# Kernel tuning notes

Measured on AMD Instinct MI355X. Metric: run time of the kernel, lower is better.

## Reference

```python
import jax, jax.numpy as jnp
import numpy as np

B, T, C = 4, 2048, 1024
H = 16
D = C // H  # head_dim = 64


def setup_inputs() -> dict:
    key = jax.random.key(0)
    ks = jax.random.split(key, 9)
    s = 1.0 / np.sqrt(C)
    return {
        "x": jax.random.normal(ks[0], (B, T, C), dtype=jnp.float32),
        "wq": jax.random.uniform(ks[1], (C, C), jnp.float32, -s, s),
        "bq": jax.random.uniform(ks[2], (C,), jnp.float32, -s, s),
        "wk": jax.random.uniform(ks[3], (C, C), jnp.float32, -s, s),
        "bk": jax.random.uniform(ks[4], (C,), jnp.float32, -s, s),
        "wv": jax.random.uniform(ks[5], (C, C), jnp.float32, -s, s),
        "bv": jax.random.uniform(ks[6], (C,), jnp.float32, -s, s),
        "wo": jax.random.uniform(ks[7], (C, C), jnp.float32, -s, s),
        "bo": jax.random.uniform(ks[8], (C,), jnp.float32, -s, s),
    }


def reference(x, wq, bq, wk, bk, wv, bv, wo, bo):
    # Linear layers (torch convention: y = x @ W.T + b)
    q = x @ wq.T + bq  # [B,T,C]
    k = x @ wk.T + bk
    v = x @ wv.T + bv
    # split heads -> [B,H,T,D]
    q = q.reshape(B, T, H, D).transpose(0, 2, 1, 3)
    k = k.reshape(B, T, H, D).transpose(0, 2, 1, 3)
    v = v.reshape(B, T, H, D).transpose(0, 2, 1, 3)
    scores = jnp.einsum('bhqd,bhkd->bhqk', q, k) / jnp.sqrt(jnp.float32(D))
    causal = jnp.tril(jnp.ones((T, T), dtype=bool))  # position i attends to j<=i
    scores = jnp.where(causal, scores, -jnp.inf)
    attn = jax.nn.softmax(scores, axis=-1)
    # dropout p=0.0 (eval / identity)
    out = jnp.einsum('bhqk,bhkd->bhqd', attn, v)  # [B,H,T,D]
    out = out.transpose(0, 2, 1, 3).reshape(B, T, C)
    return out @ wo.T + bo
```

## Files before the change

kernel.cpp:

```cpp
#include <hip/hip_runtime.h>
#include <stdint.h>

#define B_DIM 4
#define T_DIM 2048
#define C_DIM 1024
#define H_DIM 16
#define D_DIM 64
#define M_DIM (B_DIM * T_DIM)
#define QK_SCALE 0.18033688011112042f

typedef float f32x4 __attribute__((ext_vector_type(4)));
typedef float f32x16 __attribute__((ext_vector_type(16)));
typedef short bf16x8 __attribute__((ext_vector_type(8)));
typedef unsigned short u16;
typedef u16 u16x8 __attribute__((ext_vector_type(8)));

static __device__ __forceinline__ u16 f2b(float f) {
  uint32_t r;
  asm("v_cvt_pk_bf16_f32 %0, %1, %1" : "=v"(r) : "v"(f));
  return (u16)r;
}
static __device__ __forceinline__ uint32_t f2b2(float a, float b) {
  uint32_t r;
  asm("v_cvt_pk_bf16_f32 %0, %1, %2" : "=v"(r) : "v"(a), "v"(b));
  return r;
}
static __device__ __forceinline__ float xhalf_max(float x) {
  return fmaxf(x, __shfl_xor(x, 32, 64));
}
static __device__ __forceinline__ float xhalf_sum(float x) {
  return x + __shfl_xor(x, 32, 64);
}

static __device__ __forceinline__ void gl_lds16(const u16* g, u16* l) {
  __builtin_amdgcn_global_load_lds(
      (const __attribute__((address_space(1))) void*)g,
      (__attribute__((address_space(3))) void*)l, 16, 0, 0);
}

__global__ void k_cvt_all(const float* __restrict__ x,
                          const float* __restrict__ s0, const float* __restrict__ s1,
                          const float* __restrict__ s2, const float* __restrict__ s3,
                          u16* __restrict__ dx,
                          u16* __restrict__ d0, u16* __restrict__ d1,
                          u16* __restrict__ d2, u16* __restrict__ d3) {
  int i = blockIdx.x * blockDim.x + threadIdx.x;
  const float* s;
  u16* d;
  int j;
  if (i < (1 << 21)) {
    s = x; d = dx; j = i;
  } else {
    int k = i - (1 << 21);
    int seg = k >> 18;
    j = k & ((1 << 18) - 1);
    s = seg == 0 ? s0 : seg == 1 ? s1 : seg == 2 ? s2 : s3;
    d = seg == 0 ? d0 : seg == 1 ? d1 : seg == 2 ? d2 : d3;
  }
  float4 v = ((const float4*)s)[j];
  uint2 o;
  o.x = f2b2(v.x, v.y);
  o.y = f2b2(v.z, v.w);
  ((uint2*)d)[j] = o;
}

__global__ __launch_bounds__(256) void k_gemm_qkv(
    const u16* __restrict__ A,
    const u16* __restrict__ w0, const u16* __restrict__ w1, const u16* __restrict__ w2,
    const float* __restrict__ b0, const float* __restrict__ b1, const float* __restrict__ b2,
    u16* __restrict__ Qo, u16* __restrict__ Ko, u16* __restrict__ Vto) {
  __shared__ u16 As[128 * 32];
  __shared__ u16 Bs[128 * 32];
  const int tid = threadIdx.x;
  const int l = tid & 63;
  const int w = tid >> 6;
  const int wr = w >> 1, wc = w & 1;
  const int seg = blockIdx.x >> 3;
  const int brow = blockIdx.y * 128, bcol = (blockIdx.x & 7) * 128;
  const int lrow = l & 15, lk = l >> 4;
  const int K = C_DIM;

  const u16* Bw = seg == 0 ? w0 : seg == 1 ? w1 : w2;
  const float* bias = seg == 0 ? b0 : seg == 1 ? b1 : b2;
  const float scale = seg == 0 ? QK_SCALE : 1.f;

  f32x4 acc[4][4];
  for (int m = 0; m < 4; ++m)
    for (int n = 0; n < 4; ++n)
      acc[m][n] = (f32x4){0.f, 0.f, 0.f, 0.f};

  for (int kt = 0; kt < K; kt += 32) {
    __syncthreads();
    {
      int slot = tid;
      int r0 = slot >> 2, c0 = slot & 3;
      gl_lds16(A + (size_t)(brow + r0) * K + kt + c0 * 8, As + slot * 8);
      gl_lds16(Bw + (size_t)(bcol + r0) * K + kt + c0 * 8, Bs + slot * 8);
      int slot2 = slot + 256;
      int r1 = slot2 >> 2, c1 = slot2 & 3;
      gl_lds16(A + (size_t)(brow + r1) * K + kt + c1 * 8, As + slot2 * 8);
      gl_lds16(Bw + (size_t)(bcol + r1) * K + kt + c1 * 8, Bs + slot2 * 8);
    }
    asm volatile("s_waitcnt vmcnt(0)" ::: "memory");
    __syncthreads();

    bf16x8 af[4], bfr[4];
#pragma unroll
    for (int m = 0; m < 4; ++m)
      af[m] = *(const bf16x8*)(As + (wr * 64 + m * 16 + lrow) * 32 + lk * 8);
#pragma unroll
    for (int n = 0; n < 4; ++n)
      bfr[n] = *(const bf16x8*)(Bs + (wc * 64 + n * 16 + lrow) * 32 + lk * 8);
#pragma unroll
    for (int m = 0; m < 4; ++m) {
#pragma unroll
      for (int n = 0; n < 4; ++n)
        acc[m][n] = __builtin_amdgcn_mfma_f32_16x16x32_bf16(af[m], bfr[n], acc[m][n], 0, 0, 0);
    }
  }

#pragma unroll
  for (int m = 0; m < 4; ++m) {
    int rg0 = brow + wr * 64 + m * 16 + lk * 4;
    int bb = rg0 >> 11, tt0 = rg0 & (T_DIM - 1);
#pragma unroll
    for (int n = 0; n < 4; ++n) {
      int cg = bcol + wc * 64 + n * 16 + lrow;
      float bv = bias[cg];
      int hh = cg >> 6, dd = cg & 63;
      if (seg == 2) {
        float v0 = acc[m][n][0] + bv, v1 = acc[m][n][1] + bv;
        float v2 = acc[m][n][2] + bv, v3 = acc[m][n][3] + bv;
        uint2 pv;
        pv.x = f2b2(v0, v1);
        pv.y = f2b2(v2, v3);
        *(uint2*)(Vto + (((size_t)bb * H_DIM + hh) * D_DIM + dd) * T_DIM + tt0) = pv;
      } else {
        u16* Out = seg == 0 ? Qo : Ko;
#pragma unroll
        for (int i = 0; i < 4; ++i) {
          float val = (acc[m][n][i] + bv) * scale;
          Out[(((size_t)bb * H_DIM + hh) * T_DIM + tt0 + i) * D_DIM + dd] = f2b(val);
        }
      }
    }
  }
}

__global__ __launch_bounds__(256) void k_gemm_proj(
    const u16* __restrict__ A, const u16* __restrict__ Bw,
    const float* __restrict__ bias, float* __restrict__ Cout) {
  __shared__ u16 As[128 * 32];
  __shared__ u16 Bs[128 * 32];
  const int tid = threadIdx.x;
  const int l = tid & 63;
  const int w = tid >> 6;
  const int wr = w >> 1, wc = w & 1;
  const int brow = blockIdx.y * 128, bcol = blockIdx.x * 128;
  const int lrow = l & 15, lk = l >> 4;
  const int K = C_DIM, N = C_DIM;

  f32x4 acc[4][4];
  for (int m = 0; m < 4; ++m)
    for (int n = 0; n < 4; ++n)
      acc[m][n] = (f32x4){0.f, 0.f, 0.f, 0.f};

  for (int kt = 0; kt < K; kt += 32) {
    __syncthreads();
    {
      int slot = tid;
      int r0 = slot >> 2, c0 = slot & 3;
      gl_lds16(A + (size_t)(brow + r0) * K + kt + c0 * 8, As + slot * 8);
      gl_lds16(Bw + (size_t)(bcol + r0) * K + kt + c0 * 8, Bs + slot * 8);
      int slot2 = slot + 256;
      int r1 = slot2 >> 2, c1 = slot2 & 3;
      gl_lds16(A + (size_t)(brow + r1) * K + kt + c1 * 8, As + slot2 * 8);
      gl_lds16(Bw + (size_t)(bcol + r1) * K + kt + c1 * 8, Bs + slot2 * 8);
    }
    asm volatile("s_waitcnt vmcnt(0)" ::: "memory");
    __syncthreads();

    bf16x8 af[4], bfr[4];
#pragma unroll
    for (int m = 0; m < 4; ++m)
      af[m] = *(const bf16x8*)(As + (wr * 64 + m * 16 + lrow) * 32 + lk * 8);
#pragma unroll
    for (int n = 0; n < 4; ++n)
      bfr[n] = *(const bf16x8*)(Bs + (wc * 64 + n * 16 + lrow) * 32 + lk * 8);
#pragma unroll
    for (int m = 0; m < 4; ++m) {
#pragma unroll
      for (int n = 0; n < 4; ++n)
        acc[m][n] = __builtin_amdgcn_mfma_f32_16x16x32_bf16(af[m], bfr[n], acc[m][n], 0, 0, 0);
    }
  }

#pragma unroll
  for (int m = 0; m < 4; ++m) {
    int rg0 = brow + wr * 64 + m * 16 + lk * 4;
#pragma unroll
    for (int n = 0; n < 4; ++n) {
      int cg = bcol + wc * 64 + n * 16 + lrow;
      float bv = bias[cg];
#pragma unroll
      for (int i = 0; i < 4; ++i)
        Cout[(size_t)(rg0 + i) * N + cg] = acc[m][n][i] + bv;
    }
  }
}

__global__ __launch_bounds__(512) void k_attn(
    const u16* __restrict__ Q, const u16* __restrict__ Kg,
    const u16* __restrict__ Vt, u16* __restrict__ O) {
  __shared__ u16 Ks[2][128 * 64];
  __shared__ u16 Vs[2][64 * 128];

  const int tid = threadIdx.x;
  const int l = tid & 63;
  const int w = tid >> 6;
  const int id = blockIdx.x;
  const int xcd = id & 7;
  const int half = id >> 8;
  const int idh = id & 255;
  const int slot = (idh >> 3) & 7;
  const int j = idh >> 6;
  const int bh = xcd * 8 + slot;
  const int qb = half ? j : 7 - j;
  const int q0 = qb * 256;
  const int ql = l & 31;
  const int hi = l >> 5;
  const int r0 = q0 + w * 32;
  const int qg = r0 + ql;

  const size_t qkbase = (size_t)bh * T_DIM * D_DIM;
  const size_t vtbase = (size_t)bh * D_DIM * T_DIM;

  const int sr = tid >> 3, sc = tid & 7;
  const int kcol = (sc ^ (sr & 7)) * 8;
  const int vr = tid >> 4, vc = tid & 15;
  const int vcol = (vc ^ (vr & 7)) * 8;

#define STAGE(buf, kt)                                                                    \
  {                                                                                       \
    gl_lds16(Kg + qkbase + (size_t)((kt) * 128 + sr) * D_DIM + kcol, Ks[buf] + tid * 8);  \
    gl_lds16(Kg + qkbase + (size_t)((kt) * 128 + 64 + sr) * D_DIM + kcol,                 \
             Ks[buf] + 4096 + tid * 8);                                                   \
    gl_lds16(Vt + vtbase + (size_t)vr * T_DIM + (kt) * 128 + vcol, Vs[buf] + tid * 8);    \
    gl_lds16(Vt + vtbase + (size_t)(vr + 32) * T_DIM + (kt) * 128 + vcol,                 \
             Vs[buf] + 4096 + tid * 8);                                                   \
  }

  bf16x8 qf[4];
#pragma unroll
  for (int kk = 0; kk < 4; ++kk)
    qf[kk] = *(const bf16x8*)(Q + qkbase + (size_t)qg * D_DIM + kk * 16 + hi * 8);

  f32x16 oacc[2];
#pragma unroll
  for (int dt = 0; dt < 2; ++dt)
#pragma unroll
    for (int r = 0; r < 16; ++r) oacc[dt][r] = 0.f;
  float m_run = -1e30f, l_run = 0.f;

  const int tdiag64 = r0 >> 6;
  const int nkt = (q0 >> 7) + 2;

  STAGE(0, 0);

  for (int kt = 0; kt < nkt; ++kt) {
    const int cur = kt & 1;
    if (kt + 1 < nkt) {
      STAGE(cur ^ 1, kt + 1);
      asm volatile("s_waitcnt vmcnt(4)" ::: "memory");
    } else {
      asm volatile("s_waitcnt vmcnt(0)" ::: "memory");
    }
    __syncthreads();

#pragma unroll
    for (int h2 = 0; h2 < 2; ++h2) {
      const int kt64 = kt * 2 + h2;
      if (kt64 <= tdiag64) {
        const u16* Kt = Ks[cur] + h2 * 4096;
        f32x16 s[2];
#pragma unroll
        for (int a = 0; a < 2; ++a)
#pragma unroll
          for (int r = 0; r < 16; ++r) s[a][r] = 0.f;

        __builtin_amdgcn_s_setprio(1);
#pragma unroll
        for (int kk = 0; kk < 4; ++kk) {
#pragma unroll
          for (int a = 0; a < 2; ++a) {
            int row = a * 32 + ql;
            int blk = (kk * 2 + hi) ^ (row & 7);
            bf16x8 kf = *(const bf16x8*)(Kt + row * 64 + blk * 8);
            s[a] = __builtin_amdgcn_mfma_f32_32x32x16_bf16(kf, qf[kk], s[a], 0, 0, 0);
          }
        }
        __builtin_amdgcn_s_setprio(0);

        if (kt64 == tdiag64) {
#pragma unroll
          for (int a = 0; a < 2; ++a) {
#pragma unroll
            for (int r = 0; r < 16; ++r) {
              int kv = kt64 * 64 + a * 32 + (r & 3) + 8 * (r >> 2) + 4 * hi;
              if (kv > qg) s[a][r] = -1e30f;
            }
          }
        }

        float t[16];
#pragma unroll
        for (int r = 0; r < 16; ++r) t[r] = fmaxf(s[0][r], s[1][r]);
#pragma unroll
        for (int r = 0; r < 8; ++r) t[r] = fmaxf(t[r], t[r + 8]);
#pragma unroll
        for (int r = 0; r < 4; ++r) t[r] = fmaxf(t[r], t[r + 4]);
        float pm = fmaxf(fmaxf(t[0], t[1]), fmaxf(t[2], t[3]));
        pm = xhalf_max(pm);

        if (__any(pm > m_run + 8.f)) {
          float mn = fmaxf(m_run, pm);
          float sc_ = exp2f(m_run - mn);
          m_run = mn;
          l_run *= sc_;
#pragma unroll
          for (int dt = 0; dt < 2; ++dt)
#pragma unroll
            for (int r = 0; r < 16; ++r) oacc[dt][r] *= sc_;
        }

        float rs0 = 0.f, rs1 = 0.f, rs2 = 0.f, rs3 = 0.f;
#pragma unroll
        for (int a = 0; a < 2; ++a) {
#pragma unroll
          for (int r = 0; r < 16; ++r) {
            float p = exp2f(s[a][r] - m_run);
            s[a][r] = p;
            if ((r & 3) == 0) rs0 += p;
            else if ((r & 3) == 1) rs1 += p;
            else if ((r & 3) == 2) rs2 += p;
            else rs3 += p;
          }
        }
        float rs = (rs0 + rs1) + (rs2 + rs3);
        l_run += xhalf_sum(rs);

#pragma unroll
        for (int kk = 0; kk < 4; ++kk) {
          const int a = kk >> 1;
          const int base = (kk & 1) * 8;
          union { uint32_t wd[4]; bf16x8 v; } pf;
#pragma unroll
          for (int i = 0; i < 2; ++i) {
            uint32_t Aw = f2b2(s[a][base + 2 * i], s[a][base + 2 * i + 1]);
            uint32_t Bw = f2b2(s[a][base + 4 + 2 * i], s[a][base + 5 + 2 * i]);
            uint32_t As_ = (uint32_t)__shfl_xor((int)Aw, 32, 64);
            uint32_t Bs_ = (uint32_t)__shfl_xor((int)Bw, 32, 64);
            pf.wd[i] = hi ? Bs_ : Aw;
            pf.wd[2 + i] = hi ? Bw : As_;
          }
          __builtin_amdgcn_s_setprio(1);
#pragma unroll
          for (int dt = 0; dt < 2; ++dt) {
            int row = dt * 32 + ql;
            int chunk = (h2 * 8) + ((kk * 2 + hi) ^ (row & 7));
            bf16x8 vf = *(const bf16x8*)(Vs[cur] + row * 128 + chunk * 8);
            oacc[dt] = __builtin_amdgcn_mfma_f32_32x32x16_bf16(vf, pf.v, oacc[dt], 0, 0, 0);
          }
          __builtin_amdgcn_s_setprio(0);
        }
      }
    }
    __syncthreads();
  }

  const int bb = bh >> 4, hh = bh & 15;
  const float inv = 1.f / l_run;
  u16* orow = O + ((size_t)bb * T_DIM + qg) * C_DIM + hh * D_DIM;
#pragma unroll
  for (int dt = 0; dt < 2; ++dt) {
#pragma unroll
    for (int g = 0; g < 4; ++g) {
      uint2 val;
      val.x = f2b2(oacc[dt][g * 4 + 0] * inv, oacc[dt][g * 4 + 1] * inv);
      val.y = f2b2(oacc[dt][g * 4 + 2] * inv, oacc[dt][g * 4 + 3] * inv);
      *(uint2*)(orow + dt * 32 + g * 8 + 4 * hi) = val;
    }
  }
}

extern "C" void kernel_launch(void* const* d_in, const int* in_sizes, int n_in,
                              void* d_out, int out_size, void* d_ws, size_t ws_size,
                              hipStream_t stream) {
  (void)in_sizes; (void)n_in; (void)out_size; (void)ws_size;
  const float* x  = (const float*)d_in[0];
  const float* wq = (const float*)d_in[1];
  const float* bq = (const float*)d_in[2];
  const float* wk = (const float*)d_in[3];
  const float* bk = (const float*)d_in[4];
  const float* wv = (const float*)d_in[5];
  const float* bv = (const float*)d_in[6];
  const float* wo = (const float*)d_in[7];
  const float* bo = (const float*)d_in[8];
  float* out = (float*)d_out;

  u16* xb  = (u16*)d_ws;
  u16* wqb = xb + (size_t)M_DIM * C_DIM;
  u16* wkb = wqb + (size_t)C_DIM * C_DIM;
  u16* wvb = wkb + (size_t)C_DIM * C_DIM;
  u16* wob = wvb + (size_t)C_DIM * C_DIM;
  u16* Qb  = wob + (size_t)C_DIM * C_DIM;
  u16* Kb  = Qb + (size_t)M_DIM * C_DIM;
  u16* Vtb = Kb + (size_t)M_DIM * C_DIM;
  u16* Ob  = Vtb + (size_t)M_DIM * C_DIM;

  k_cvt_all<<<12288, 256, 0, stream>>>(x, wq, wk, wv, wo, xb, wqb, wkb, wvb, wob);

  k_gemm_qkv<<<dim3(24, M_DIM / 128), 256, 0, stream>>>(
      xb, wqb, wkb, wvb, bq, bk, bv, Qb, Kb, Vtb);

  k_attn<<<512, 512, 0, stream>>>(Qb, Kb, Vtb, Ob);
  k_gemm_proj<<<dim3(C_DIM / 128, M_DIM / 128), 256, 0, stream>>>(Ob, wob, bo, out);
}
```

Measured before the change: 194.4 us.

## Software-pipeline QK of second sub-tile ahead of PV of first in attention

Restructures the attention inner loop so the QK^T MFMAs for the second 64-key sub-tile are issued before the PV MFMAs of the first sub-tile, letting the softmax work of one sub-tile overlap matrix work of the other. The per-sub-tile logic is factored into lambdas without changing the math. It also adds a min-blocks hint of 4 to launch bounds, which caps register use and may cause spills, since holding two score tiles at once raises register pressure.

```diff
diff --git a/kernel.cpp b/kernel.cpp
--- a/kernel.cpp
+++ b/kernel.cpp
@@ -209,7 +209,7 @@
   }
 }
 
-__global__ __launch_bounds__(512) void k_attn(
+__global__ __launch_bounds__(512, 4) void k_attn(
     const u16* __restrict__ Q, const u16* __restrict__ Kg,
     const u16* __restrict__ Vt, u16* __restrict__ O) {
   __shared__ u16 Ks[2][128 * 64];
@@ -265,6 +265,104 @@
   const int tdiag64 = r0 >> 6;
   const int nkt = (q0 >> 7) + 2;
 
+  auto QK_SUB = [&](f32x16* sarr, const u16* Kt) {
+    __builtin_amdgcn_s_setprio(1);
+#pragma unroll
+    for (int kk = 0; kk < 4; ++kk) {
+#pragma unroll
+      for (int a = 0; a < 2; ++a) {
+        int row = a * 32 + ql;
+        int blk = (kk * 2 + hi) ^ (row & 7);
+        bf16x8 kf = *(const bf16x8*)(Kt + row * 64 + blk * 8);
+        sarr[a] = __builtin_amdgcn_mfma_f32_32x32x16_bf16(kf, qf[kk], sarr[a], 0, 0, 0);
+      }
+    }
+    __builtin_amdgcn_s_setprio(0);
+  };
+
+  auto SM_SUB = [&](f32x16* sarr, int kt64) {
+    if (kt64 == tdiag64) {
+#pragma unroll
+      for (int a = 0; a < 2; ++a) {
+#pragma unroll
+        for (int r = 0; r < 16; ++r) {
+          int kv = kt64 * 64 + a * 32 + (r & 3) + 8 * (r >> 2) + 4 * hi;
+          if (kv > qg) sarr[a][r] = -1e30f;
+        }
+      }
+    }
+    float t[16];
+#pragma unroll
+    for (int r = 0; r < 16; ++r) t[r] = fmaxf(sarr[0][r], sarr[1][r]);
+#pragma unroll
+    for (int r = 0; r < 8; ++r) t[r] = fmaxf(t[r], t[r + 8]);
+#pragma unroll
+    for (int r = 0; r < 4; ++r) t[r] = fmaxf(t[r], t[r + 4]);
+    float pm = fmaxf(fmaxf(t[0], t[1]), fmaxf(t[2], t[3]));
+    pm = xhalf_max(pm);
+
+    if (__any(pm > m_run + 8.f)) {
+      float mn = fmaxf(m_run, pm);
+      float sc_ = exp2f(m_run - mn);
+      m_run = mn;
+      l_run *= sc_;
+#pragma unroll
+      for (int dt = 0; dt < 2; ++dt)
+#pragma unroll
+        for (int r = 0; r < 16; ++r) oacc[dt][r] *= sc_;
+    }
+
+    float rs0 = 0.f, rs1 = 0.f, rs2 = 0.f, rs3 = 0.f;
+#pragma unroll
+    for (int a = 0; a < 2; ++a) {
+#pragma unroll
+      for (int r = 0; r < 16; ++r) {
+        float p = exp2f(sarr[a][r] - m_run);
+        sarr[a][r] = p;
+        if ((r & 3) == 0) rs0 += p;
+        else if ((r & 3) == 1) rs1 += p;
+        else if ((r & 3) == 2) rs2 += p;
+        else rs3 += p;
+      }
+    }
+    float rs = (rs0 + rs1) + (rs2 + rs3);
+    l_run += xhalf_sum(rs);
+  };
+
+  auto PF_BUILD = [&](const f32x16* sarr, bf16x8* pf) {
+#pragma unroll
+    for (int kk = 0; kk < 4; ++kk) {
+      const int a = kk >> 1;
+      const int base = (kk & 1) * 8;
+      union { uint32_t wd[4]; bf16x8 v; } u;
+#pragma unroll
+      for (int i = 0; i < 2; ++i) {
+        uint32_t Aw = f2b2(sarr[a][base + 2 * i], sarr[a][base + 2 * i + 1]);
+        uint32_t Bw = f2b2(sarr[a][base + 4 + 2 * i], sarr[a][base + 5 + 2 * i]);
+        uint32_t As_ = (uint32_t)__shfl_xor((int)Aw, 32, 64);
+        uint32_t Bs_ = (uint32_t)__shfl_xor((int)Bw, 32, 64);
+        u.wd[i] = hi ? Bs_ : Aw;
+        u.wd[2 + i] = hi ? Bw : As_;
+      }
+      pf[kk] = u.v;
+    }
+  };
+
+  auto PV_SUB = [&](const bf16x8* pf, int h2, int cur) {
+    __builtin_amdgcn_s_setprio(1);
+#pragma unroll
+    for (int kk = 0; kk < 4; ++kk) {
+#pragma unroll
+      for (int dt = 0; dt < 2; ++dt) {
+        int row = dt * 32 + ql;
+        int chunk = (h2 * 8) + ((kk * 2 + hi) ^ (row & 7));
+        bf16x8 vf = *(const bf16x8*)(Vs[cur] + row * 128 + chunk * 8);
+        oacc[dt] = __builtin_amdgcn_mfma_f32_32x32x16_bf16(vf, pf[kk], oacc[dt], 0, 0, 0);
+      }
+    }
+    __builtin_amdgcn_s_setprio(0);
+  };
+
   STAGE(0, 0);
 
   for (int kt = 0; kt < nkt; ++kt) {
@@ -277,102 +375,38 @@
     }
     __syncthreads();
 
-#pragma unroll
-    for (int h2 = 0; h2 < 2; ++h2) {
-      const int kt64 = kt * 2 + h2;
-      if (kt64 <= tdiag64) {
-        const u16* Kt = Ks[cur] + h2 * 4096;
-        f32x16 s[2];
+    const int kt64_0 = kt * 2;
+    const int kt64_1 = kt * 2 + 1;
+    const bool v0 = (kt64_0 <= tdiag64);
+    const bool v1 = (kt64_1 <= tdiag64);
+
+    if (v0) {
+      f32x16 s0[2];
+#pragma unroll
+      for (int a = 0; a < 2; ++a)
+#pragma unroll
+        for (int r = 0; r < 16; ++r) s0[a][r] = 0.f;
+
+      QK_SUB(s0, Ks[cur]);
+      SM_SUB(s0, kt64_0);
+      bf16x8 pf0[4];
+      PF_BUILD(s0, pf0);
+
+      if (v1) {
+        f32x16 s1[2];
 #pragma unroll
         for (int a = 0; a < 2; ++a)
 #pragma unroll
-          for (int r = 0; r < 16; ++r) s[a][r] = 0.f;
-
-        __builtin_amdgcn_s_setprio(1);
-#pragma unroll
-        for (int kk = 0; kk < 4; ++kk) {
-#pragma unroll
-          for (int a = 0; a < 2; ++a) {
-            int row = a * 32 + ql;
-            int blk = (kk * 2 + hi) ^ (row & 7);
-            bf16x8 kf = *(const bf16x8*)(Kt + row * 64 + blk * 8);
-            s[a] = __builtin_amdgcn_mfma_f32_32x32x16_bf16(kf, qf[kk], s[a], 0, 0, 0);
-          }
-        }
-        __builtin_amdgcn_s_setprio(0);
-
-        if (kt64 == tdiag64) {
-#pragma unroll
-          for (int a = 0; a < 2; ++a) {
-#pragma unroll
-            for (int r = 0; r < 16; ++r) {
-              int kv = kt64 * 64 + a * 32 + (r & 3) + 8 * (r >> 2) + 4 * hi;
-              if (kv > qg) s[a][r] = -1e30f;
-            }
-          }
-        }
-
-        float t[16];
-#pragma unroll
-        for (int r = 0; r < 16; ++r) t[r] = fmaxf(s[0][r], s[1][r]);
-#pragma unroll
-        for (int r = 0; r < 8; ++r) t[r] = fmaxf(t[r], t[r + 8]);
-#pragma unroll
-        for (int r = 0; r < 4; ++r) t[r] = fmaxf(t[r], t[r + 4]);
-        float pm = fmaxf(fmaxf(t[0], t[1]), fmaxf(t[2], t[3]));
-        pm = xhalf_max(pm);
-
-        if (__any(pm > m_run + 8.f)) {
-          float mn = fmaxf(m_run, pm);
-          float sc_ = exp2f(m_run - mn);
-          m_run = mn;
-          l_run *= sc_;
-#pragma unroll
-          for (int dt = 0; dt < 2; ++dt)
-#pragma unroll
-            for (int r = 0; r < 16; ++r) oacc[dt][r] *= sc_;
-        }
-
-        float rs0 = 0.f, rs1 = 0.f, rs2 = 0.f, rs3 = 0.f;
-#pragma unroll
-        for (int a = 0; a < 2; ++a) {
-#pragma unroll
-          for (int r = 0; r < 16; ++r) {
-            float p = exp2f(s[a][r] - m_run);
-            s[a][r] = p;
-            if ((r & 3) == 0) rs0 += p;
-            else if ((r & 3) == 1) rs1 += p;
-            else if ((r & 3) == 2) rs2 += p;
-            else rs3 += p;
-          }
-        }
-        float rs = (rs0 + rs1) + (rs2 + rs3);
-        l_run += xhalf_sum(rs);
-
-#pragma unroll
-        for (int kk = 0; kk < 4; ++kk) {
-          const int a = kk >> 1;
-          const int base = (kk & 1) * 8;
-          union { uint32_t wd[4]; bf16x8 v; } pf;
-#pragma unroll
-          for (int i = 0; i < 2; ++i) {
-            uint32_t Aw = f2b2(s[a][base + 2 * i], s[a][base + 2 * i + 1]);
-            uint32_t Bw = f2b2(s[a][base + 4 + 2 * i], s[a][base + 5 + 2 * i]);
-            uint32_t As_ = (uint32_t)__shfl_xor((int)Aw, 32, 64);
-            uint32_t Bs_ = (uint32_t)__shfl_xor((int)Bw, 32, 64);
-            pf.wd[i] = hi ? Bs_ : Aw;
-            pf.wd[2 + i] = hi ? Bw : As_;
-          }
-          __builtin_amdgcn_s_setprio(1);
-#pragma unroll
-          for (int dt = 0; dt < 2; ++dt) {
-            int row = dt * 32 + ql;
-            int chunk = (h2 * 8) + ((kk * 2 + hi) ^ (row & 7));
-            bf16x8 vf = *(const bf16x8*)(Vs[cur] + row * 128 + chunk * 8);
-            oacc[dt] = __builtin_amdgcn_mfma_f32_32x32x16_bf16(vf, pf.v, oacc[dt], 0, 0, 0);
-          }
-          __builtin_amdgcn_s_setprio(0);
-        }
+          for (int r = 0; r < 16; ++r) s1[a][r] = 0.f;
+
+        QK_SUB(s1, Ks[cur] + 4096);
+        PV_SUB(pf0, 0, cur);
+        SM_SUB(s1, kt64_1);
+        bf16x8 pf1[4];
+        PF_BUILD(s1, pf1);
+        PV_SUB(pf1, 1, cur);
+      } else {
+        PV_SUB(pf0, 0, cur);
       }
     }
     __syncthreads();
```

After: 198.7 us. +2.2%, slower.
